# Kernel optimization log

Hardware: AMD Instinct MI355X
Metric: run time of the kernel (lower is better)

## Reference

```python
import jax, jax.numpy as jnp
import numpy as np

N, E, B = 102400, 1638400, 512
DIN, DH, DG = 64, 100, 20
D2, D3 = 200, 300
DF, R, AH, GH, H1, H2, DOUT = 64, 8, 128, 128, 128, 32, 1
EPS = 1e-5


def _xavier(k, i, o):
    lim = float(np.sqrt(6.0 / (i + o)))
    return jax.random.uniform(k, (i, o), minval=-lim, maxval=lim, dtype=jnp.float32)


def setup_inputs() -> dict:
    key = jax.random.key(0)
    ks = jax.random.split(key, 32)
    inp = {
        'node_feat': jax.random.normal(ks[0], (N, DIN), dtype=jnp.float32),
        'self_feat': jax.random.normal(ks[1], (B, D2), dtype=jnp.float32),
        'x3d': jax.random.normal(ks[2], (B, D3), dtype=jnp.float32),
        'src': jax.random.randint(ks[3], (E,), 0, N, dtype=jnp.int32),
        'dst': jax.random.randint(ks[4], (E,), 0, N, dtype=jnp.int32),
        'graph_id': (jnp.arange(N, dtype=jnp.int32) // (N // B)),
        # GCN params (weights stored (in, out))
        'gc1_w': _xavier(ks[5], DIN, DH), 'gc1_b': jnp.zeros((DH,), jnp.float32),
        'gc2_w': _xavier(ks[6], DH, DG), 'gc2_b': jnp.zeros((DG,), jnp.float32),
        # modality gate MLP
        'gate_w1': _xavier(ks[7], DG + D2 + D3, GH), 'gate_b1': jnp.zeros((GH,), jnp.float32),
        'gate_w2': _xavier(ks[8], GH, 3), 'gate_b2': jnp.zeros((3,), jnp.float32),
        # fusion projections + layernorms
        'pg_w': _xavier(ks[9], DG, DF), 'pg_b': jnp.zeros((DF,), jnp.float32),
        'p2_w': _xavier(ks[10], D2, DF), 'p2_b': jnp.zeros((DF,), jnp.float32),
        'p3_w': _xavier(ks[11], D3, DF), 'p3_b': jnp.zeros((DF,), jnp.float32),
        'lng_g': jnp.ones((DF,), jnp.float32), 'lng_b': jnp.zeros((DF,), jnp.float32),
        'ln2_g': jnp.ones((DF,), jnp.float32), 'ln2_b': jnp.zeros((DF,), jnp.float32),
        'ln3_g': jnp.ones((DF,), jnp.float32), 'ln3_b': jnp.zeros((DF,), jnp.float32),
        # low-rank CP factors
        'U_w': _xavier(ks[12], DF, R * DF),
        'V_w': _xavier(ks[13], DF, R * DF),
        'S_w': _xavier(ks[14], DF, R * DF),
        # rank attention MLP
        'attn_w1': _xavier(ks[15], DG + D2 + D3, AH), 'attn_b1': jnp.zeros((AH,), jnp.float32),
        'attn_w2': _xavier(ks[16], AH, R), 'attn_b2': jnp.zeros((R,), jnp.float32),
        # head MLP + batchnorms (training-mode batch stats)
        'fc1_w': _xavier(ks[17], DF, H1), 'fc1_b': jnp.zeros((H1,), jnp.float32),
        'fc2_w': _xavier(ks[18], H1, H2), 'fc2_b': jnp.zeros((H2,), jnp.float32),
        'fc3_w': _xavier(ks[19], H2, DOUT), 'fc3_b': jnp.zeros((DOUT,), jnp.float32),
        'bn1_g': jnp.ones((H1,), jnp.float32), 'bn1_b': jnp.zeros((H1,), jnp.float32),
        'bn2_g': jnp.ones((H2,), jnp.float32), 'bn2_b': jnp.zeros((H2,), jnp.float32),
    }
    return inp


def _gcn(h, src, dst, w, b):
    n = h.shape[0]
    msg = jax.ops.segment_sum(h[src], dst, num_segments=n)           # gather + scatter-add
    deg = jax.ops.segment_sum(jnp.ones((src.shape[0],), h.dtype), dst, num_segments=n)
    agg = msg / jnp.maximum(deg, 1.0)[:, None]                       # mean over mailbox
    return agg @ w + b


def _ln(x, g, b):
    mu = jnp.mean(x, axis=-1, keepdims=True)
    var = jnp.mean(jnp.square(x - mu), axis=-1, keepdims=True)
    return g * (x - mu) * jax.lax.rsqrt(var + EPS) + b


def _bn(x, g, b):
    mu = jnp.mean(x, axis=0)
    var = jnp.mean(jnp.square(x - mu), axis=0)
    return g * (x - mu) * jax.lax.rsqrt(var + EPS) + b


def reference(node_feat, self_feat, x3d, src, dst, graph_id,
              gc1_w, gc1_b, gc2_w, gc2_b,
              gate_w1, gate_b1, gate_w2, gate_b2,
              pg_w, pg_b, p2_w, p2_b, p3_w, p3_b,
              lng_g, lng_b, ln2_g, ln2_b, ln3_g, ln3_b,
              U_w, V_w, S_w,
              attn_w1, attn_b1, attn_w2, attn_b2,
              fc1_w, fc1_b, fc2_w, fc2_b, fc3_w, fc3_b,
              bn1_g, bn1_b, bn2_g, bn2_b):
    b = self_feat.shape[0]
    # two GCN layers (copy_u + mean reduce + linear), relu
    h = jax.nn.relu(_gcn(node_feat, src, dst, gc1_w, gc1_b))
    h = jax.nn.relu(_gcn(h, src, dst, gc2_w, gc2_b))
    # dgl.mean_nodes: per-graph mean readout
    cnt = jax.ops.segment_sum(jnp.ones((h.shape[0],), h.dtype), graph_id, num_segments=b)
    hg = jax.ops.segment_sum(h, graph_id, num_segments=b) / cnt[:, None]  # (B, DG)
    # modality gate
    cat = jnp.concatenate([hg, self_feat, x3d], axis=-1)
    alpha = jax.nn.softmax(jax.nn.relu(cat @ gate_w1 + gate_b1) @ gate_w2 + gate_b2, axis=-1)
    hg2 = hg * alpha[:, 0:1]
    sf2 = self_feat * alpha[:, 1:2]
    x3d2 = x3d * alpha[:, 2:3]
    # low-rank tri-linear fusion with rank attention (dropout = identity, eval mode)
    gp = jax.nn.relu(_ln(hg2 @ pg_w + pg_b, lng_g, lng_b))
    d2 = jax.nn.relu(_ln(sf2 @ p2_w + p2_b, ln2_g, ln2_b))
    d3 = jax.nn.relu(_ln(x3d2 @ p3_w + p3_b, ln3_g, ln3_b))
    g_r = (gp @ U_w).reshape(b, R, DF)
    d2_r = (d2 @ V_w).reshape(b, R, DF)
    d3_r = (d3 @ S_w).reshape(b, R, DF)
    z_r = g_r * d2_r * d3_r                                          # (B, R, DF)
    cat2 = jnp.concatenate([hg2, sf2, x3d2], axis=-1)
    beta = jax.nn.softmax(jax.nn.relu(cat2 @ attn_w1 + attn_b1) @ attn_w2 + attn_b2, axis=-1)
    z = jnp.sum(z_r * beta[:, :, None], axis=1)                      # (B, DF)
    # head MLP with batchnorm (batch statistics)
    out = jax.nn.relu(_bn(z @ fc1_w + fc1_b, bn1_g, bn1_b))
    out = jax.nn.relu(_bn(out @ fc2_w + fc2_b, bn2_g, bn2_b))
    out = out @ fc3_w + fc3_b
    return out
```

## Files before the change

kernel.cpp:

```cpp
#include <hip/hip_runtime.h>

#define N_NODES 102400
#define N_EDGES 1638400
#define BB 512
#define DIN 64
#define DH 100
#define DG 20
#define D2 200
#define D3 300
#define DF 64
#define RR 8
#define H1 128
#define H2 32
#define NPG (N_NODES / BB)
#define EPSV 1e-5f
#define CAP 48
#define TB6 6
#define NSLICE 8
#define SLICEN (N_NODES / NSLICE)
#define EBLK 6400
#define SEGC 64
#define PAIRS_S (EBLK * SEGC)
#define SUBN 400
#define TROWS 2

typedef float v2f __attribute__((ext_vector_type(2)));
typedef unsigned v4u __attribute__((ext_vector_type(4)));

__device__ __forceinline__ float wave_sum64(float v) {
#pragma unroll
    for (int m = 32; m >= 1; m >>= 1) v += __shfl_xor(v, m, 64);
    return v;
}

__device__ __forceinline__ unsigned enc4_fp8(float x0, float x1, float x2, float x3) {
    int r = __builtin_amdgcn_cvt_pk_fp8_f32(x0, x1, 0, false);
    r = __builtin_amdgcn_cvt_pk_fp8_f32(x2, x3, r, true);
    return (unsigned)r;
}
__device__ __forceinline__ void dec8_acc2(uint2 w, v2f* a) {
    a[0] += __builtin_amdgcn_cvt_pk_f32_fp8((int)w.x, false);
    a[1] += __builtin_amdgcn_cvt_pk_f32_fp8((int)w.x, true);
    a[2] += __builtin_amdgcn_cvt_pk_f32_fp8((int)w.y, false);
    a[3] += __builtin_amdgcn_cvt_pk_f32_fp8((int)w.y, true);
}
__device__ __forceinline__ unsigned short f2bf(float x) {
    unsigned u = __float_as_uint(x);
    u += 0x7fffu + ((u >> 16) & 1u);
    return (unsigned short)(u >> 16);
}
__device__ __forceinline__ float bf2f(unsigned u16) {
    return __uint_as_float(u16 << 16);
}

__global__ __launch_bounds__(256) void prep(
    const float* __restrict__ nf, unsigned* __restrict__ nfb,
    const int* __restrict__ src, const int* __restrict__ dst,
    unsigned* __restrict__ pairs) {
    __shared__ int binCnt[NSLICE];
    int b = blockIdx.x, t = threadIdx.x;
    if (b < 6400) {
        int i = b * 256 + t;
        float4 v = ((const float4*)nf)[i];
        nfb[i] = enc4_fp8(v.x, v.y, v.z, v.w);
    } else {
        int idx = b - 6400;
        int e = idx * 256 + t;
        int d = __builtin_nontemporal_load(&dst[e]);
        int s = __builtin_nontemporal_load(&src[e]);
        int slice = d / SLICEN;
        unsigned code = ((unsigned)(d - slice * SLICEN) << 17) | (unsigned)s;
        if (t < NSLICE) binCnt[t] = 0;
        for (int q = t; q < NSLICE * SEGC; q += 256)
            pairs[(size_t)(q >> 6) * PAIRS_S + idx * SEGC + (q & 63)] = 0xFFFFFFFFu;
        __syncthreads();
        int loc = atomicAdd(&binCnt[slice], 1);
        if (loc < SEGC)
            pairs[(size_t)slice * PAIRS_S + idx * SEGC + loc] = code;
    }
}

__global__ __launch_bounds__(1024) void bucket(
    const unsigned* __restrict__ pairs,
    int* __restrict__ counts, int* __restrict__ col) {
    __shared__ int cnt[SUBN];
    int b = blockIdx.x, t = threadIdx.x;
    int s = b & 7, j = b >> 3;
    int dlo = j * SUBN;
    int lo = s * SLICEN;
    if (t < SUBN) cnt[t] = 0;
    __syncthreads();
    const v4u* p4 = (const v4u*)(pairs + (size_t)s * PAIRS_S);
    for (int k = 0; k < PAIRS_S / 4096; k++) {
        v4u w = __builtin_nontemporal_load(&p4[k * 1024 + t]);
#pragma unroll
        for (int q = 0; q < 4; q++) {
            unsigned code = w[q];
            int dl = (int)(code >> 17);
            unsigned rel = (unsigned)(dl - dlo);
            if (rel < (unsigned)SUBN) {
                int pos = atomicAdd(&cnt[rel], 1);
                if (pos < CAP) col[(lo + dl) * CAP + pos] = (int)(code & 0x1FFFFu);
            }
        }
    }
    __syncthreads();
    if (t < SUBN) counts[lo + dlo + t] = cnt[t];
}

__global__ __launch_bounds__(512) void agg_gather(
    const unsigned* __restrict__ nfb, const int* __restrict__ counts,
    const int* __restrict__ col, unsigned short* __restrict__ aggb) {
    const uint2* nfb2 = (const uint2*)nfb;
    int t = threadIdx.x;
    int wid = t >> 6, l = t & 63;
    int h = l >> 5, hl = l & 31;
    int o = hl & 7;
    int g = hl >> 3;
    int hb = 32 * h;
    int n = blockIdx.x * 16 + wid * 2 + h;
    int cnt = counts[n]; if (cnt > CAP) cnt = CAP;
    int cmax = max(cnt, __shfl_xor(cnt, 32, 64));
    v2f a2[4];
#pragma unroll
    for (int j = 0; j < 4; j++) { a2[j].x = 0.f; a2[j].y = 0.f; }
    int idx = (hl < cnt) ? __builtin_nontemporal_load(&col[n * CAP + hl]) : 0;
    int nIt = (min(cmax, 32) + 3) >> 2;
    int m = 0;
    for (; m + 1 < nIt; m += 2) {
        int e0 = m * 4 + g, e1 = (m + 1) * 4 + g;
        int k0 = max(min(e0, cnt - 1), 0);
        int k1 = max(min(e1, cnt - 1), 0);
        int s0 = __shfl(idx, hb + k0, 64);
        int s1 = __shfl(idx, hb + k1, 64);
        uint2 v0 = nfb2[(size_t)s0 * 8 + o];
        uint2 v1 = nfb2[(size_t)s1 * 8 + o];
        if (e0 < cnt) dec8_acc2(v0, a2);
        if (e1 < cnt) dec8_acc2(v1, a2);
    }
    if (m < nIt) {
        int e0 = m * 4 + g;
        int k0 = max(min(e0, cnt - 1), 0);
        int s0 = __shfl(idx, hb + k0, 64);
        uint2 v0 = nfb2[(size_t)s0 * 8 + o];
        if (e0 < cnt) dec8_acc2(v0, a2);
    }
    if (cmax > 32) {
        int idx_hi = (hl < 16 && 32 + hl < cnt)
                   ? __builtin_nontemporal_load(&col[n * CAP + 32 + hl]) : 0;
#pragma unroll
        for (int mm2 = 0; mm2 < 4; mm2++) {
            int e = 32 + mm2 * 4 + g;
            int kk = max(min(e, cnt - 1), 0);
            int kLo = (kk < 32) ? kk : 0;
            int kHi = (kk >= 32) ? (kk - 32) : 0;
            int sL = __shfl(idx, hb + kLo, 64);
            int sH = __shfl(idx_hi, hb + kHi, 64);
            int s = (kk >= 32) ? sH : sL;
            uint2 v = nfb2[(size_t)s * 8 + o];
            if (e < cnt) dec8_acc2(v, a2);
        }
    }
#pragma unroll
    for (int mm = 8; mm <= 16; mm <<= 1) {
#pragma unroll
        for (int j = 0; j < 4; j++) {
            v2f oth;
            oth.x = __shfl_xor(a2[j].x, mm, 64);
            oth.y = __shfl_xor(a2[j].y, mm, 64);
            a2[j] += oth;
        }
    }
    if (hl < 8) {
        float inv = 1.0f / fmaxf((float)cnt, 1.0f);
        float av[8] = {a2[0].x, a2[0].y, a2[1].x, a2[1].y,
                       a2[2].x, a2[2].y, a2[3].x, a2[3].y};
        unsigned us[8];
#pragma unroll
        for (int j = 0; j < 8; j++) us[j] = (unsigned)f2bf(av[j] * inv);
        uint4 w;
        w.x = us[0] | (us[1] << 16);
        w.y = us[2] | (us[3] << 16);
        w.z = us[4] | (us[5] << 16);
        w.w = us[6] | (us[7] << 16);
        *(uint4*)(aggb + (size_t)n * 64 + 8 * hl) = w;
    }
}

__global__ __launch_bounds__(256) void w12(
    const unsigned short* __restrict__ aggb,
    const float* __restrict__ w1, const float* __restrict__ b1,
    const float* __restrict__ w2, unsigned* __restrict__ tb) {
    __shared__ float smem[64 * 101];
    int b = blockIdx.x, t = threadIdx.x;
    int n0 = b * 64;
    const uint4* ag4 = (const uint4*)(aggb + (size_t)n0 * 64);
#pragma unroll
    for (int k = 0; k < 2; k++) {
        int q = t + k * 256;
        uint4 w = ag4[q];
        int row = q >> 3, c8 = (q & 7) * 8;
        float* sa = &smem[row * 65 + c8];
        sa[0] = bf2f(w.x & 0xffffu); sa[1] = bf2f(w.x >> 16);
        sa[2] = bf2f(w.y & 0xffffu); sa[3] = bf2f(w.y >> 16);
        sa[4] = bf2f(w.z & 0xffffu); sa[5] = bf2f(w.z >> 16);
        sa[6] = bf2f(w.w & 0xffffu); sa[7] = bf2f(w.w >> 16);
    }
    __syncthreads();
    int lane = t & 63;
    int c0 = __builtin_amdgcn_readfirstlane((t >> 6) * 25);
    float acc[25];
#pragma unroll
    for (int cc = 0; cc < 25; cc++) acc[cc] = b1[c0 + cc];
    for (int i = 0; i < DIN; i++) {
        float x = smem[lane * 65 + i];
        const float* wr = &w1[i * DH + c0];
#pragma unroll
        for (int cc = 0; cc < 25; cc++) acc[cc] += x * wr[cc];
    }
    __syncthreads();
#pragma unroll
    for (int cc = 0; cc < 25; cc++)
        smem[lane * 101 + c0 + cc] = fmaxf(acc[cc], 0.f);
    __syncthreads();
    for (int task = t; task < 320; task += 256) {
        int j = task / 5, p = task % 5;
        float a0 = 0.f, a1 = 0.f, a2 = 0.f, a3 = 0.f;
        for (int i = 0; i < DH; i++) {
            float hv = smem[j * 101 + i];
            float4 w = *(const float4*)&w2[i * DG + 4 * p];
            a0 += hv * w.x; a1 += hv * w.y; a2 += hv * w.z; a3 += hv * w.w;
        }
        tb[(size_t)(n0 + j) * TB6 + p] = enc4_fp8(a0, a1, a2, a3);
    }
    if (t < 64) tb[(size_t)(n0 + t) * TB6 + 5] = 0u;
}

__global__ __launch_bounds__(512) void gcn2_gather(
    const unsigned* __restrict__ tb, const int* __restrict__ counts,
    const int* __restrict__ col,
    const float* __restrict__ b2, float* __restrict__ hg) {
    const uint2* tb2 = (const uint2*)tb;
    int t = threadIdx.x;
    int wid = t >> 6, l = t & 63;
    int h = l >> 5, hl = l & 31;
    int o = hl & 3;
    int g = hl >> 2;
    int hb = 32 * h;
    int n = blockIdx.x * 16 + wid * 2 + h;
    int cnt = counts[n]; if (cnt > CAP) cnt = CAP;
    int cmax = max(cnt, __shfl_xor(cnt, 32, 64));
    bool ok = (o < 3);
    uint2 zz = make_uint2(0u, 0u);
    v2f a2[4];
#pragma unroll
    for (int j = 0; j < 4; j++) { a2[j].x = 0.f; a2[j].y = 0.f; }
    int idx = (hl < cnt) ? __builtin_nontemporal_load(&col[n * CAP + hl]) : 0;
    int nIt = (min(cmax, 32) + 7) >> 3;
    int m = 0;
    for (; m + 1 < nIt; m += 2) {
        int e0 = m * 8 + g, e1 = (m + 1) * 8 + g;
        int k0 = max(min(e0, cnt - 1), 0);
        int k1 = max(min(e1, cnt - 1), 0);
        int s0 = __shfl(idx, hb + k0, 64);
        int s1 = __shfl(idx, hb + k1, 64);
        uint2 v0 = ok ? tb2[(size_t)s0 * 3 + o] : zz;
        uint2 v1 = ok ? tb2[(size_t)s1 * 3 + o] : zz;
        if (e0 < cnt) dec8_acc2(v0, a2);
        if (e1 < cnt) dec8_acc2(v1, a2);
    }
    if (m < nIt) {
        int e0 = m * 8 + g;
        int k0 = max(min(e0, cnt - 1), 0);
        int s0 = __shfl(idx, hb + k0, 64);
        uint2 v0 = ok ? tb2[(size_t)s0 * 3 + o] : zz;
        if (e0 < cnt) dec8_acc2(v0, a2);
    }
    if (cmax > 32) {
        int idx_hi = (hl < 16 && 32 + hl < cnt)
                   ? __builtin_nontemporal_load(&col[n * CAP + 32 + hl]) : 0;
#pragma unroll
        for (int mm2 = 0; mm2 < 2; mm2++) {
            int e = 32 + mm2 * 8 + g;
            int kk = max(min(e, cnt - 1), 0);
            int kLo = (kk < 32) ? kk : 0;
            int kHi = (kk >= 32) ? (kk - 32) : 0;
            int sL = __shfl(idx, hb + kLo, 64);
            int sH = __shfl(idx_hi, hb + kHi, 64);
            int s = (kk >= 32) ? sH : sL;
            uint2 v = ok ? tb2[(size_t)s * 3 + o] : zz;
            if (e < cnt) dec8_acc2(v, a2);
        }
    }
#pragma unroll
    for (int mm = 4; mm <= 16; mm <<= 1) {
#pragma unroll
        for (int j = 0; j < 4; j++) {
            v2f oth;
            oth.x = __shfl_xor(a2[j].x, mm, 64);
            oth.y = __shfl_xor(a2[j].y, mm, 64);
            a2[j] += oth;
        }
    }
    __shared__ float red[16][DG];
    int nb = t >> 5;
    if (hl < 3) {
        float inv = 1.0f / fmaxf((float)cnt, 1.0f);
        float av[8] = {a2[0].x, a2[0].y, a2[1].x, a2[1].y,
                       a2[2].x, a2[2].y, a2[3].x, a2[3].y};
#pragma unroll
        for (int j = 0; j < 8; j++) {
            int f = 8 * hl + j;
            if (f < DG) red[nb][f] = fmaxf(av[j] * inv + b2[f], 0.f);
        }
    }
    __syncthreads();
    if (t < 2 * DG) {
        int half = t / DG, f = t % DG;
        float s = 0.f;
#pragma unroll
        for (int j = 0; j < 8; j++) s += red[half * 8 + j][f];
        int gid = (blockIdx.x * 16 + half * 8) / NPG;
        atomicAdd(&hg[gid * DG + f], s * (1.0f / (float)NPG));
    }
}

__device__ __forceinline__ float ln_relu(float x, float g, float b) {
    float mu = wave_sum64(x) * (1.0f / DF);
    float d = x - mu;
    float var = wave_sum64(d * d) * (1.0f / DF);
    float v = g * d * rsqrtf(var + EPSV) + b;
    return fmaxf(v, 0.f);
}

__global__ __launch_bounds__(512) void row_tail(
    const float* __restrict__ hg, const float* __restrict__ sf, const float* __restrict__ x3,
    const float* __restrict__ gate_w1, const float* __restrict__ gate_b1,
    const float* __restrict__ gate_w2, const float* __restrict__ gate_b2,
    const float* __restrict__ attn_w1, const float* __restrict__ attn_b1,
    const float* __restrict__ attn_w2, const float* __restrict__ attn_b2,
    const float* __restrict__ pg_w, const float* __restrict__ pg_b,
    const float* __restrict__ p2_w, const float* __restrict__ p2_b,
    const float* __restrict__ p3_w, const float* __restrict__ p3_b,
    const float* __restrict__ lng_g, const float* __restrict__ lng_b,
    const float* __restrict__ ln2_g, const float* __restrict__ ln2_b,
    const float* __restrict__ ln3_g, const float* __restrict__ ln3_b,
    const float* __restrict__ U_w, const float* __restrict__ V_w, const float* __restrict__ S_w,
    const float* __restrict__ fc1_w, const float* __restrict__ fc1_b,
    float* __restrict__ y1) {
    int r0 = blockIdx.x * TROWS, t = threadIdx.x;
    __shared__ float s_in[TROWS][DG + D2 + D3];
    __shared__ float s_part[1024];
    __shared__ float s_hid[TROWS][128];
    __shared__ float s_sm[TROWS][RR];
    __shared__ float s_alpha[TROWS][3];
    __shared__ float s_beta[TROWS][RR];
    __shared__ float s_raw[3][TROWS][DF];
    __shared__ float s_gp[TROWS][DF], s_d2[TROWS][DF], s_d3[TROWS][DF], s_z[TROWS][DF];

    for (int q = t; q < TROWS * 520; q += 512) {
        int r = q / 520, i = q % 520;
        s_in[r][i] = (i < DG) ? hg[(r0 + r) * DG + i]
                   : (i < DG + D2) ? sf[(r0 + r) * D2 + (i - DG)]
                   : x3[(r0 + r) * D3 + (i - DG - D2)];
    }
    __syncthreads();

    {
        int c = t & 127, ks = t >> 7, k0 = ks * 130;
        float a0 = 0.f, a1 = 0.f;
        for (int i = k0; i < k0 + 130; i++) {
            float w = gate_w1[i * 128 + c];
            a0 += s_in[0][i] * w; a1 += s_in[1][i] * w;
        }
        s_part[(ks * 2 + 0) * 128 + c] = a0;
        s_part[(ks * 2 + 1) * 128 + c] = a1;
    }
    __syncthreads();
    if (t < 256) {
        int r = t >> 7, c = t & 127;
        float h = s_part[(0 + r) * 128 + c] + s_part[(2 + r) * 128 + c]
                + s_part[(4 + r) * 128 + c] + s_part[(6 + r) * 128 + c] + gate_b1[c];
        s_hid[r][c] = fmaxf(h, 0.f);
    }
    __syncthreads();
    if (t < TROWS * 3) {
        int r = t / 3, j = t % 3;
        float p = gate_b2[j];
        for (int i = 0; i < 128; i++) p += s_hid[r][i] * gate_w2[i * 3 + j];
        s_sm[r][j] = p;
    }
    __syncthreads();
    if (t < TROWS) {
        float mx = fmaxf(s_sm[t][0], fmaxf(s_sm[t][1], s_sm[t][2]));
        float e0 = __expf(s_sm[t][0] - mx), e1 = __expf(s_sm[t][1] - mx), e2 = __expf(s_sm[t][2] - mx);
        float inv = 1.0f / (e0 + e1 + e2);
        s_alpha[t][0] = e0 * inv; s_alpha[t][1] = e1 * inv; s_alpha[t][2] = e2 * inv;
    }
    __syncthreads();
    for (int q = t; q < TROWS * 520; q += 512) {
        int r = q / 520, i = q % 520;
        float sc = (i < DG) ? s_alpha[r][0] : (i < DG + D2) ? s_alpha[r][1] : s_alpha[r][2];
        s_in[r][i] *= sc;
    }
    __syncthreads();

    {
        int c = t & 127, ks = t >> 7, k0 = ks * 130;
        float a0 = 0.f, a1 = 0.f;
        for (int i = k0; i < k0 + 130; i++) {
            float w = attn_w1[i * 128 + c];
            a0 += s_in[0][i] * w; a1 += s_in[1][i] * w;
        }
        s_part[(ks * 2 + 0) * 128 + c] = a0;
        s_part[(ks * 2 + 1) * 128 + c] = a1;
    }
    __syncthreads();
    if (t < 256) {
        int r = t >> 7, c = t & 127;
        float h = s_part[(0 + r) * 128 + c] + s_part[(2 + r) * 128 + c]
                + s_part[(4 + r) * 128 + c] + s_part[(6 + r) * 128 + c] + attn_b1[c];
        s_hid[r][c] = fmaxf(h, 0.f);
    }
    __syncthreads();
    if (t < TROWS * RR) {
        int r = t / RR, j = t % RR;
        float p = attn_b2[j];
        for (int i = 0; i < 128; i++) p += s_hid[r][i] * attn_w2[i * RR + j];
        s_sm[r][j] = p;
    }
    __syncthreads();
    if (t < TROWS) {
        float mx = -1e30f;
#pragma unroll
        for (int k = 0; k < RR; k++) mx = fmaxf(mx, s_sm[t][k]);
        float se = 0.f, e[RR];
#pragma unroll
        for (int k = 0; k < RR; k++) { e[k] = __expf(s_sm[t][k] - mx); se += e[k]; }
        float inv = 1.0f / se;
#pragma unroll
        for (int k = 0; k < RR; k++) s_beta[t][k] = e[k] * inv;
    }
    if (t < TROWS * DF) {
        int r = t >> 6, c = t & 63;
        float a = pg_b[c];
        for (int i = 0; i < DG; i++) a += s_in[r][i] * pg_w[i * DF + c];
        s_raw[0][r][c] = a;
    }
    {
        int ks = t >> 6, c = t & 63, k0 = ks * 25;
        float a0 = 0.f, a1 = 0.f;
        for (int u = 0; u < 25; u++) {
            float w = p2_w[(k0 + u) * DF + c];
            a0 += s_in[0][DG + k0 + u] * w; a1 += s_in[1][DG + k0 + u] * w;
        }
        s_part[(ks * 2 + 0) * 64 + c] = a0;
        s_part[(ks * 2 + 1) * 64 + c] = a1;
    }
    __syncthreads();
    if (t < TROWS * DF) {
        int r = t >> 6, c = t & 63;
        float a = p2_b[c];
#pragma unroll
        for (int ks = 0; ks < 8; ks++) a += s_part[(ks * 2 + r) * 64 + c];
        s_raw[1][r][c] = a;
    }
    __syncthreads();
    {
        int ks = t >> 6, c = t & 63;
        int k0 = (ks * 300) >> 3, k1 = ((ks + 1) * 300) >> 3;
        float a0 = 0.f, a1 = 0.f;
        for (int i = k0; i < k1; i++) {
            float w = p3_w[i * DF + c];
            a0 += s_in[0][DG + D2 + i] * w; a1 += s_in[1][DG + D2 + i] * w;
        }
        s_part[(ks * 2 + 0) * 64 + c] = a0;
        s_part[(ks * 2 + 1) * 64 + c] = a1;
    }
    __syncthreads();
    if (t < TROWS * DF) {
        int r = t >> 6, c = t & 63;
        float a = p3_b[c];
#pragma unroll
        for (int ks = 0; ks < 8; ks++) a += s_part[(ks * 2 + r) * 64 + c];
        s_gp[r][c] = ln_relu(s_raw[0][r][c], lng_g[c], lng_b[c]);
        s_d2[r][c] = ln_relu(s_raw[1][r][c], ln2_g[c], ln2_b[c]);
        s_d3[r][c] = ln_relu(a, ln3_g[c], ln3_b[c]);
    }
    __syncthreads();

    {
        int rr = t >> 6, f = t & 63;
        float u0 = 0.f, u1 = 0.f, v0 = 0.f, v1 = 0.f, w0 = 0.f, w1 = 0.f;
        for (int i = 0; i < DF; i++) {
            float uw = U_w[i * (RR * DF) + rr * DF + f];
            float vw = V_w[i * (RR * DF) + rr * DF + f];
            float sw = S_w[i * (RR * DF) + rr * DF + f];
            u0 += s_gp[0][i] * uw; u1 += s_gp[1][i] * uw;
            v0 += s_d2[0][i] * vw; v1 += s_d2[1][i] * vw;
            w0 += s_d3[0][i] * sw; w1 += s_d3[1][i] * sw;
        }
        s_part[(rr * 2 + 0) * 64 + f] = s_beta[0][rr] * u0 * v0 * w0;
        s_part[(rr * 2 + 1) * 64 + f] = s_beta[1][rr] * u1 * v1 * w1;
    }
    __syncthreads();
    if (t < TROWS * DF) {
        int r = t >> 6, f = t & 63;
        float z = 0.f;
#pragma unroll
        for (int rr = 0; rr < 8; rr++) z += s_part[(rr * 2 + r) * 64 + f];
        s_z[r][f] = z;
    }
    __syncthreads();

    {
        int c = t & 127, ks = t >> 7, k0 = ks * 16;
        float a0 = 0.f, a1 = 0.f;
        for (int i = k0; i < k0 + 16; i++) {
            float w = fc1_w[i * H1 + c];
            a0 += s_z[0][i] * w; a1 += s_z[1][i] * w;
        }
        s_part[(ks * 2 + 0) * 128 + c] = a0;
        s_part[(ks * 2 + 1) * 128 + c] = a1;
    }
    __syncthreads();
    if (t < 256) {
        int r = t >> 7, c = t & 127;
        float a = fc1_b[c];
#pragma unroll
        for (int ks = 0; ks < 4; ks++) a += s_part[(ks * 2 + r) * 128 + c];
        y1[(r0 + r) * H1 + c] = a;
    }
}

__global__ __launch_bounds__(256) void head2(
    const float* __restrict__ y1,
    const float* __restrict__ bn1_g, const float* __restrict__ bn1_b,
    const float* __restrict__ fc2_w, const float* __restrict__ fc2_b,
    float* __restrict__ y2) {
    int row = blockIdx.x, t = threadIdx.x;
    __shared__ float sp[2][H1], sp2[2][H1];
    int h = t >> 7, c = t & 127;
    float s = 0.f, s2 = 0.f;
#pragma unroll 8
    for (int r = h * 256; r < h * 256 + 256; r++) {
        float v = y1[r * H1 + c];
        s += v; s2 += v * v;
    }
    sp[h][c] = s; sp2[h][c] = s2;
    __syncthreads();
    __shared__ float sh[H1];
    if (t < H1) {
        float S = sp[0][t] + sp[1][t];
        float S2 = sp2[0][t] + sp2[1][t];
        float m = S * (1.0f / BB);
        float ri = rsqrtf(S2 * (1.0f / BB) - m * m + EPSV);
        float v = y1[row * H1 + t];
        sh[t] = fmaxf(bn1_g[t] * (v - m) * ri + bn1_b[t], 0.f);
    }
    __syncthreads();
    if (t < H2) {
        float acc = fc2_b[t];
        for (int i = 0; i < H1; i++) acc += sh[i] * fc2_w[i * H2 + t];
        y2[row * H2 + t] = acc;
    }
}

__global__ __launch_bounds__(256) void head3(
    const float* __restrict__ y2,
    const float* __restrict__ bn2_g, const float* __restrict__ bn2_b,
    const float* __restrict__ fc3_w, const float* __restrict__ fc3_b,
    float* __restrict__ out) {
    int t = threadIdx.x;
    __shared__ float smu[H2], sri[H2];
    if (t < H2) {
        float s = 0.f, s2 = 0.f;
#pragma unroll 8
        for (int r = 0; r < BB; r++) {
            float v = y2[r * H2 + t];
            s += v; s2 += v * v;
        }
        float m = s * (1.0f / BB);
        smu[t] = m;
        sri[t] = rsqrtf(s2 * (1.0f / BB) - m * m + EPSV);
    }
    __syncthreads();
    int row = blockIdx.x * 256 + t;
    float acc = fc3_b[0];
    for (int i = 0; i < H2; i++) {
        float v = y2[row * H2 + i];
        v = bn2_g[i] * (v - smu[i]) * sri[i] + bn2_b[i];
        acc += fmaxf(v, 0.f) * fc3_w[i];
    }
    out[row] = acc;
}

extern "C" void kernel_launch(void* const* d_in, const int* in_sizes, int n_in,
                              void* d_out, int out_size, void* d_ws, size_t ws_size,
                              hipStream_t stream) {
    const float* node_feat = (const float*)d_in[0];
    const float* self_feat = (const float*)d_in[1];
    const float* x3d       = (const float*)d_in[2];
    const int*   src       = (const int*)d_in[3];
    const int*   dst       = (const int*)d_in[4];
    const float* gc1_w = (const float*)d_in[6];
    const float* gc1_b = (const float*)d_in[7];
    const float* gc2_w = (const float*)d_in[8];
    const float* gc2_b = (const float*)d_in[9];
    const float* gate_w1 = (const float*)d_in[10];
    const float* gate_b1 = (const float*)d_in[11];
    const float* gate_w2 = (const float*)d_in[12];
    const float* gate_b2 = (const float*)d_in[13];
    const float* pg_w = (const float*)d_in[14];
    const float* pg_b = (const float*)d_in[15];
    const float* p2_w = (const float*)d_in[16];
    const float* p2_b = (const float*)d_in[17];
    const float* p3_w = (const float*)d_in[18];
    const float* p3_b = (const float*)d_in[19];
    const float* lng_g = (const float*)d_in[20];
    const float* lng_b = (const float*)d_in[21];
    const float* ln2_g = (const float*)d_in[22];
    const float* ln2_b = (const float*)d_in[23];
    const float* ln3_g = (const float*)d_in[24];
    const float* ln3_b = (const float*)d_in[25];
    const float* U_w = (const float*)d_in[26];
    const float* V_w = (const float*)d_in[27];
    const float* S_w = (const float*)d_in[28];
    const float* attn_w1 = (const float*)d_in[29];
    const float* attn_b1 = (const float*)d_in[30];
    const float* attn_w2 = (const float*)d_in[31];
    const float* attn_b2 = (const float*)d_in[32];
    const float* fc1_w = (const float*)d_in[33];
    const float* fc1_b = (const float*)d_in[34];
    const float* fc2_w = (const float*)d_in[35];
    const float* fc2_b = (const float*)d_in[36];
    const float* fc3_w = (const float*)d_in[37];
    const float* fc3_b = (const float*)d_in[38];
    const float* bn1_g = (const float*)d_in[39];
    const float* bn1_b = (const float*)d_in[40];
    const float* bn2_g = (const float*)d_in[41];
    const float* bn2_b = (const float*)d_in[42];

    char* base = (char*)d_ws;
    int* counts   = (int*)base;                      base += sizeof(int) * N_NODES;
    int* col      = (int*)base;                      base += sizeof(int) * (size_t)N_NODES * CAP;
    unsigned* nfb = (unsigned*)base;                 base += sizeof(unsigned) * (size_t)N_NODES * 16;
    unsigned* tb  = (unsigned*)base;                 base += sizeof(unsigned) * (size_t)N_NODES * TB6;
    unsigned short* aggb = (unsigned short*)base;    base += sizeof(unsigned short) * (size_t)N_NODES * 64;
    float* hg    = (float*)base;                     base += sizeof(float) * BB * DG;
    float* y1    = (float*)base;                     base += sizeof(float) * BB * H1;
    float* y2    = (float*)base;                     base += sizeof(float) * BB * H2;
    float* outf  = (float*)d_out;
    unsigned* pairs = (unsigned*)aggb;

    hipMemsetAsync(hg, 0, sizeof(float) * BB * DG, stream);

    prep<<<6400 + EBLK, 256, 0, stream>>>(node_feat, nfb, src, dst, pairs);
    bucket<<<256, 1024, 0, stream>>>(pairs, counts, col);

    agg_gather<<<N_NODES / 16, 512, 0, stream>>>(nfb, counts, col, aggb);
    w12<<<N_NODES / 64, 256, 0, stream>>>(aggb, gc1_w, gc1_b, gc2_w, tb);
    gcn2_gather<<<N_NODES / 16, 512, 0, stream>>>(tb, counts, col, gc2_b, hg);

    row_tail<<<BB / TROWS, 512, 0, stream>>>(hg, self_feat, x3d,
                                     gate_w1, gate_b1, gate_w2, gate_b2,
                                     attn_w1, attn_b1, attn_w2, attn_b2,
                                     pg_w, pg_b, p2_w, p2_b, p3_w, p3_b,
                                     lng_g, lng_b, ln2_g, ln2_b, ln3_g, ln3_b,
                                     U_w, V_w, S_w, fc1_w, fc1_b, y1);
    head2<<<BB, 256, 0, stream>>>(y1, bn1_g, bn1_b, fc2_w, fc2_b, y2);
    head3<<<BB / 256, 256, 0, stream>>>(y2, bn2_g, bn2_b, fc3_w, fc3_b, outf);
}
```

Before: 413.5 us.

## Split bucket pass across pair halves and widen row_tail to 1024 threads

The bucket kernel now has each block handle 800 destination nodes over half of the edge-pair stream. The two halves fill col from opposite ends and merge their counts with packed 16-bit atomics into a zeroed counts array. The gather kernels unpack the two counts and remap slots around the gap between them. row_tail moves to 1024 threads with finer K splits so each block does less serial work per thread. The cost is an extra memset, the atomics, and extra index arithmetic in the gathers.

```diff
diff --git a/kernel.cpp b/kernel.cpp
--- a/kernel.cpp
+++ b/kernel.cpp
@@ -21,7 +21,7 @@
 #define EBLK 6400
 #define SEGC 64
 #define PAIRS_S (EBLK * SEGC)
-#define SUBN 400
+#define SUBN 800
 #define TROWS 2
 
 typedef float v2f __attribute__((ext_vector_type(2)));
@@ -51,6 +51,14 @@
 }
 __device__ __forceinline__ float bf2f(unsigned u16) {
     return __uint_as_float(u16 << 16);
+}
+
+__device__ __forceinline__ void cnt_unpack(int w, int& cnt0, int& cnt) {
+    cnt0 = w & 0xffff;
+    int cnt1 = (w >> 16) & 0xffff;
+    if (cnt0 > CAP) cnt0 = CAP;
+    if (cnt1 > CAP - cnt0) cnt1 = CAP - cnt0;
+    cnt = cnt0 + cnt1;
 }
 
 __global__ __launch_bounds__(256) void prep(
@@ -85,13 +93,15 @@
     int* __restrict__ counts, int* __restrict__ col) {
     __shared__ int cnt[SUBN];
     int b = blockIdx.x, t = threadIdx.x;
-    int s = b & 7, j = b >> 3;
+    int s = b & 7;
+    int u = b >> 3;
+    int j = u & 15, h = u >> 4;
     int dlo = j * SUBN;
     int lo = s * SLICEN;
-    if (t < SUBN) cnt[t] = 0;
-    __syncthreads();
-    const v4u* p4 = (const v4u*)(pairs + (size_t)s * PAIRS_S);
-    for (int k = 0; k < PAIRS_S / 4096; k++) {
+    for (int q = t; q < SUBN; q += 1024) cnt[q] = 0;
+    __syncthreads();
+    const v4u* p4 = (const v4u*)(pairs + (size_t)s * PAIRS_S + (size_t)h * (PAIRS_S / 2));
+    for (int k = 0; k < (PAIRS_S / 2) / 4096; k++) {
         v4u w = __builtin_nontemporal_load(&p4[k * 1024 + t]);
 #pragma unroll
         for (int q = 0; q < 4; q++) {
@@ -100,12 +110,16 @@
             unsigned rel = (unsigned)(dl - dlo);
             if (rel < (unsigned)SUBN) {
                 int pos = atomicAdd(&cnt[rel], 1);
-                if (pos < CAP) col[(lo + dl) * CAP + pos] = (int)(code & 0x1FFFFu);
+                if (pos < CAP) {
+                    int slot = h ? (CAP - 1 - pos) : pos;
+                    col[(lo + dl) * CAP + slot] = (int)(code & 0x1FFFFu);
+                }
             }
         }
     }
     __syncthreads();
-    if (t < SUBN) counts[lo + dlo + t] = cnt[t];
+    for (int q = t; q < SUBN; q += 1024)
+        atomicAdd(&counts[lo + dlo + q], cnt[q] << (16 * h));
 }
 
 __global__ __launch_bounds__(512) void agg_gather(
@@ -119,12 +133,15 @@
     int g = hl >> 3;
     int hb = 32 * h;
     int n = blockIdx.x * 16 + wid * 2 + h;
-    int cnt = counts[n]; if (cnt > CAP) cnt = CAP;
+    int cnt0, cnt;
+    cnt_unpack(counts[n], cnt0, cnt);
+    int gap = CAP - cnt;
     int cmax = max(cnt, __shfl_xor(cnt, 32, 64));
     v2f a2[4];
 #pragma unroll
     for (int j = 0; j < 4; j++) { a2[j].x = 0.f; a2[j].y = 0.f; }
-    int idx = (hl < cnt) ? __builtin_nontemporal_load(&col[n * CAP + hl]) : 0;
+    int slot0 = (hl < cnt0) ? hl : hl + gap;
+    int idx = (hl < cnt) ? __builtin_nontemporal_load(&col[n * CAP + slot0]) : 0;
     int nIt = (min(cmax, 32) + 3) >> 2;
     int m = 0;
     for (; m + 1 < nIt; m += 2) {
@@ -146,8 +163,10 @@
         if (e0 < cnt) dec8_acc2(v0, a2);
     }
     if (cmax > 32) {
-        int idx_hi = (hl < 16 && 32 + hl < cnt)
-                   ? __builtin_nontemporal_load(&col[n * CAP + 32 + hl]) : 0;
+        int e32 = 32 + hl;
+        int slotH = (e32 < cnt0) ? e32 : e32 + gap;
+        int idx_hi = (hl < 16 && e32 < cnt)
+                   ? __builtin_nontemporal_load(&col[n * CAP + slotH]) : 0;
 #pragma unroll
         for (int mm2 = 0; mm2 < 4; mm2++) {
             int e = 32 + mm2 * 4 + g;
@@ -248,14 +267,17 @@
     int g = hl >> 2;
     int hb = 32 * h;
     int n = blockIdx.x * 16 + wid * 2 + h;
-    int cnt = counts[n]; if (cnt > CAP) cnt = CAP;
+    int cnt0, cnt;
+    cnt_unpack(counts[n], cnt0, cnt);
+    int gap = CAP - cnt;
     int cmax = max(cnt, __shfl_xor(cnt, 32, 64));
     bool ok = (o < 3);
     uint2 zz = make_uint2(0u, 0u);
     v2f a2[4];
 #pragma unroll
     for (int j = 0; j < 4; j++) { a2[j].x = 0.f; a2[j].y = 0.f; }
-    int idx = (hl < cnt) ? __builtin_nontemporal_load(&col[n * CAP + hl]) : 0;
+    int slot0 = (hl < cnt0) ? hl : hl + gap;
+    int idx = (hl < cnt) ? __builtin_nontemporal_load(&col[n * CAP + slot0]) : 0;
     int nIt = (min(cmax, 32) + 7) >> 3;
     int m = 0;
     for (; m + 1 < nIt; m += 2) {
@@ -277,8 +299,10 @@
         if (e0 < cnt) dec8_acc2(v0, a2);
     }
     if (cmax > 32) {
-        int idx_hi = (hl < 16 && 32 + hl < cnt)
-                   ? __builtin_nontemporal_load(&col[n * CAP + 32 + hl]) : 0;
+        int e32 = 32 + hl;
+        int slotH = (e32 < cnt0) ? e32 : e32 + gap;
+        int idx_hi = (hl < 16 && e32 < cnt)
+                   ? __builtin_nontemporal_load(&col[n * CAP + slotH]) : 0;
 #pragma unroll
         for (int mm2 = 0; mm2 < 2; mm2++) {
             int e = 32 + mm2 * 8 + g;
@@ -333,7 +357,7 @@
     return fmaxf(v, 0.f);
 }
 
-__global__ __launch_bounds__(512) void row_tail(
+__global__ __launch_bounds__(1024) void row_tail(
     const float* __restrict__ hg, const float* __restrict__ sf, const float* __restrict__ x3,
     const float* __restrict__ gate_w1, const float* __restrict__ gate_b1,
     const float* __restrict__ gate_w2, const float* __restrict__ gate_b2,
@@ -350,15 +374,15 @@
     float* __restrict__ y1) {
     int r0 = blockIdx.x * TROWS, t = threadIdx.x;
     __shared__ float s_in[TROWS][DG + D2 + D3];
-    __shared__ float s_part[1024];
+    __shared__ float s_part[2048];
     __shared__ float s_hid[TROWS][128];
     __shared__ float s_sm[TROWS][RR];
     __shared__ float s_alpha[TROWS][3];
     __shared__ float s_beta[TROWS][RR];
-    __shared__ float s_raw[3][TROWS][DF];
+    __shared__ float s_raw[2][TROWS][DF];
     __shared__ float s_gp[TROWS][DF], s_d2[TROWS][DF], s_d3[TROWS][DF], s_z[TROWS][DF];
 
-    for (int q = t; q < TROWS * 520; q += 512) {
+    for (int q = t; q < TROWS * 520; q += 1024) {
         int r = q / 520, i = q % 520;
         s_in[r][i] = (i < DG) ? hg[(r0 + r) * DG + i]
                    : (i < DG + D2) ? sf[(r0 + r) * D2 + (i - DG)]
@@ -367,9 +391,9 @@
     __syncthreads();
 
     {
-        int c = t & 127, ks = t >> 7, k0 = ks * 130;
+        int c = t & 127, ks = t >> 7, k0 = ks * 65;
         float a0 = 0.f, a1 = 0.f;
-        for (int i = k0; i < k0 + 130; i++) {
+        for (int i = k0; i < k0 + 65; i++) {
             float w = gate_w1[i * 128 + c];
             a0 += s_in[0][i] * w; a1 += s_in[1][i] * w;
         }
@@ -379,9 +403,10 @@
     __syncthreads();
     if (t < 256) {
         int r = t >> 7, c = t & 127;
-        float h = s_part[(0 + r) * 128 + c] + s_part[(2 + r) * 128 + c]
-                + s_part[(4 + r) * 128 + c] + s_part[(6 + r) * 128 + c] + gate_b1[c];
-        s_hid[r][c] = fmaxf(h, 0.f);
+        float hsum = gate_b1[c];
+#pragma unroll
+        for (int ks = 0; ks < 8; ks++) hsum += s_part[(ks * 2 + r) * 128 + c];
+        s_hid[r][c] = fmaxf(hsum, 0.f);
     }
     __syncthreads();
     if (t < TROWS * 3) {
@@ -398,7 +423,7 @@
         s_alpha[t][0] = e0 * inv; s_alpha[t][1] = e1 * inv; s_alpha[t][2] = e2 * inv;
     }
     __syncthreads();
-    for (int q = t; q < TROWS * 520; q += 512) {
+    for (int q = t; q < TROWS * 520; q += 1024) {
         int r = q / 520, i = q % 520;
         float sc = (i < DG) ? s_alpha[r][0] : (i < DG + D2) ? s_alpha[r][1] : s_alpha[r][2];
         s_in[r][i] *= sc;
@@ -406,9 +431,9 @@
     __syncthreads();
 
     {
-        int c = t & 127, ks = t >> 7, k0 = ks * 130;
+        int c = t & 127, ks = t >> 7, k0 = ks * 65;
         float a0 = 0.f, a1 = 0.f;
-        for (int i = k0; i < k0 + 130; i++) {
+        for (int i = k0; i < k0 + 65; i++) {
             float w = attn_w1[i * 128 + c];
             a0 += s_in[0][i] * w; a1 += s_in[1][i] * w;
         }
@@ -418,9 +443,10 @@
     __syncthreads();
     if (t < 256) {
         int r = t >> 7, c = t & 127;
-        float h = s_part[(0 + r) * 128 + c] + s_part[(2 + r) * 128 + c]
-                + s_part[(4 + r) * 128 + c] + s_part[(6 + r) * 128 + c] + attn_b1[c];
-        s_hid[r][c] = fmaxf(h, 0.f);
+        float hsum = attn_b1[c];
+#pragma unroll
+        for (int ks = 0; ks < 8; ks++) hsum += s_part[(ks * 2 + r) * 128 + c];
+        s_hid[r][c] = fmaxf(hsum, 0.f);
     }
     __syncthreads();
     if (t < TROWS * RR) {
@@ -448,11 +474,12 @@
         s_raw[0][r][c] = a;
     }
     {
-        int ks = t >> 6, c = t & 63, k0 = ks * 25;
+        int ks = t >> 6, c = t & 63;
+        int k0 = (ks * 200) >> 4, k1 = ((ks + 1) * 200) >> 4;
         float a0 = 0.f, a1 = 0.f;
-        for (int u = 0; u < 25; u++) {
-            float w = p2_w[(k0 + u) * DF + c];
-            a0 += s_in[0][DG + k0 + u] * w; a1 += s_in[1][DG + k0 + u] * w;
+        for (int i = k0; i < k1; i++) {
+            float w = p2_w[i * DF + c];
+            a0 += s_in[0][DG + i] * w; a1 += s_in[1][DG + i] * w;
         }
         s_part[(ks * 2 + 0) * 64 + c] = a0;
         s_part[(ks * 2 + 1) * 64 + c] = a1;
@@ -462,13 +489,13 @@
         int r = t >> 6, c = t & 63;
         float a = p2_b[c];
 #pragma unroll
-        for (int ks = 0; ks < 8; ks++) a += s_part[(ks * 2 + r) * 64 + c];
+        for (int ks = 0; ks < 16; ks++) a += s_part[(ks * 2 + r) * 64 + c];
         s_raw[1][r][c] = a;
     }
     __syncthreads();
     {
         int ks = t >> 6, c = t & 63;
-        int k0 = (ks * 300) >> 3, k1 = ((ks + 1) * 300) >> 3;
+        int k0 = (ks * 300) >> 4, k1 = ((ks + 1) * 300) >> 4;
         float a0 = 0.f, a1 = 0.f;
         for (int i = k0; i < k1; i++) {
             float w = p3_w[i * DF + c];
@@ -482,7 +509,7 @@
         int r = t >> 6, c = t & 63;
         float a = p3_b[c];
 #pragma unroll
-        for (int ks = 0; ks < 8; ks++) a += s_part[(ks * 2 + r) * 64 + c];
+        for (int ks = 0; ks < 16; ks++) a += s_part[(ks * 2 + r) * 64 + c];
         s_gp[r][c] = ln_relu(s_raw[0][r][c], lng_g[c], lng_b[c]);
         s_d2[r][c] = ln_relu(s_raw[1][r][c], ln2_g[c], ln2_b[c]);
         s_d3[r][c] = ln_relu(a, ln3_g[c], ln3_b[c]);
@@ -490,18 +517,14 @@
     __syncthreads();
 
     {
-        int rr = t >> 6, f = t & 63;
-        float u0 = 0.f, u1 = 0.f, v0 = 0.f, v1 = 0.f, w0 = 0.f, w1 = 0.f;
+        int row = t >> 9, rr = (t >> 6) & 7, f = t & 63;
+        float gu = 0.f, dv = 0.f, ds = 0.f;
         for (int i = 0; i < DF; i++) {
-            float uw = U_w[i * (RR * DF) + rr * DF + f];
-            float vw = V_w[i * (RR * DF) + rr * DF + f];
-            float sw = S_w[i * (RR * DF) + rr * DF + f];
-            u0 += s_gp[0][i] * uw; u1 += s_gp[1][i] * uw;
-            v0 += s_d2[0][i] * vw; v1 += s_d2[1][i] * vw;
-            w0 += s_d3[0][i] * sw; w1 += s_d3[1][i] * sw;
-        }
-        s_part[(rr * 2 + 0) * 64 + f] = s_beta[0][rr] * u0 * v0 * w0;
-        s_part[(rr * 2 + 1) * 64 + f] = s_beta[1][rr] * u1 * v1 * w1;
+            gu += s_gp[row][i] * U_w[i * (RR * DF) + rr * DF + f];
+            dv += s_d2[row][i] * V_w[i * (RR * DF) + rr * DF + f];
+            ds += s_d3[row][i] * S_w[i * (RR * DF) + rr * DF + f];
+        }
+        s_part[(rr * 2 + row) * 64 + f] = s_beta[row][rr] * gu * dv * ds;
     }
     __syncthreads();
     if (t < TROWS * DF) {
@@ -514,9 +537,9 @@
     __syncthreads();
 
     {
-        int c = t & 127, ks = t >> 7, k0 = ks * 16;
+        int c = t & 127, ks = t >> 7, k0 = ks * 8;
         float a0 = 0.f, a1 = 0.f;
-        for (int i = k0; i < k0 + 16; i++) {
+        for (int i = k0; i < k0 + 8; i++) {
             float w = fc1_w[i * H1 + c];
             a0 += s_z[0][i] * w; a1 += s_z[1][i] * w;
         }
@@ -528,7 +551,7 @@
         int r = t >> 7, c = t & 127;
         float a = fc1_b[c];
 #pragma unroll
-        for (int ks = 0; ks < 4; ks++) a += s_part[(ks * 2 + r) * 128 + c];
+        for (int ks = 0; ks < 8; ks++) a += s_part[(ks * 2 + r) * 128 + c];
         y1[(r0 + r) * H1 + c] = a;
     }
 }
@@ -653,6 +676,7 @@
     float* outf  = (float*)d_out;
     unsigned* pairs = (unsigned*)aggb;
 
+    hipMemsetAsync(counts, 0, sizeof(int) * N_NODES, stream);
     hipMemsetAsync(hg, 0, sizeof(float) * BB * DG, stream);
 
     prep<<<6400 + EBLK, 256, 0, stream>>>(node_feat, nfb, src, dst, pairs);
@@ -662,7 +686,7 @@
     w12<<<N_NODES / 64, 256, 0, stream>>>(aggb, gc1_w, gc1_b, gc2_w, tb);
     gcn2_gather<<<N_NODES / 16, 512, 0, stream>>>(tb, counts, col, gc2_b, hg);
 
-    row_tail<<<BB / TROWS, 512, 0, stream>>>(hg, self_feat, x3d,
+    row_tail<<<BB / TROWS, 1024, 0, stream>>>(hg, self_feat, x3d,
                                      gate_w1, gate_b1, gate_w2, gate_b2,
                                      attn_w1, attn_b1, attn_w2, attn_b2,
                                      pg_w, pg_b, p2_w, p2_b, p3_w, p3_b,
```

Result: no change. 407.7 us (-1.4%).

## Split bucket pass into two half-scans per slice with packed counts

Applied to the files above, without the earlier changes.

The bucket kernel now covers 800 destinations per block and splits each slice's pair stream into two halves, handled by separate blocks. The first half fills column slots from the front and the second from the back, and each half's count goes into 16 bits of a packed counter merged with atomics. The gather kernels unpack both counts and remap slot indices around the gap. This halves the number of times each pair segment is re-read across blocks (from 16 to 8 scans per slice) while keeping the same block count. In exchange it needs a memset of the counts buffer, global atomics, and extra index arithmetic in both gathers.

```diff
diff --git a/kernel.cpp b/kernel.cpp
--- a/kernel.cpp
+++ b/kernel.cpp
@@ -21,7 +21,7 @@
 #define EBLK 6400
 #define SEGC 64
 #define PAIRS_S (EBLK * SEGC)
-#define SUBN 400
+#define SUBN 800
 #define TROWS 2
 
 typedef float v2f __attribute__((ext_vector_type(2)));
@@ -51,6 +51,14 @@
 }
 __device__ __forceinline__ float bf2f(unsigned u16) {
     return __uint_as_float(u16 << 16);
+}
+
+__device__ __forceinline__ void cnt_unpack(int w, int& cnt0, int& cnt) {
+    cnt0 = w & 0xffff;
+    int cnt1 = (w >> 16) & 0xffff;
+    if (cnt0 > CAP) cnt0 = CAP;
+    if (cnt1 > CAP - cnt0) cnt1 = CAP - cnt0;
+    cnt = cnt0 + cnt1;
 }
 
 __global__ __launch_bounds__(256) void prep(
@@ -85,13 +93,15 @@
     int* __restrict__ counts, int* __restrict__ col) {
     __shared__ int cnt[SUBN];
     int b = blockIdx.x, t = threadIdx.x;
-    int s = b & 7, j = b >> 3;
+    int s = b & 7;
+    int u = b >> 3;
+    int j = u & 15, h = u >> 4;
     int dlo = j * SUBN;
     int lo = s * SLICEN;
-    if (t < SUBN) cnt[t] = 0;
-    __syncthreads();
-    const v4u* p4 = (const v4u*)(pairs + (size_t)s * PAIRS_S);
-    for (int k = 0; k < PAIRS_S / 4096; k++) {
+    for (int q = t; q < SUBN; q += 1024) cnt[q] = 0;
+    __syncthreads();
+    const v4u* p4 = (const v4u*)(pairs + (size_t)s * PAIRS_S + (size_t)h * (PAIRS_S / 2));
+    for (int k = 0; k < (PAIRS_S / 2) / 4096; k++) {
         v4u w = __builtin_nontemporal_load(&p4[k * 1024 + t]);
 #pragma unroll
         for (int q = 0; q < 4; q++) {
@@ -100,12 +110,16 @@
             unsigned rel = (unsigned)(dl - dlo);
             if (rel < (unsigned)SUBN) {
                 int pos = atomicAdd(&cnt[rel], 1);
-                if (pos < CAP) col[(lo + dl) * CAP + pos] = (int)(code & 0x1FFFFu);
+                if (pos < CAP) {
+                    int slot = h ? (CAP - 1 - pos) : pos;
+                    col[(lo + dl) * CAP + slot] = (int)(code & 0x1FFFFu);
+                }
             }
         }
     }
     __syncthreads();
-    if (t < SUBN) counts[lo + dlo + t] = cnt[t];
+    for (int q = t; q < SUBN; q += 1024)
+        atomicAdd(&counts[lo + dlo + q], cnt[q] << (16 * h));
 }
 
 __global__ __launch_bounds__(512) void agg_gather(
@@ -119,12 +133,15 @@
     int g = hl >> 3;
     int hb = 32 * h;
     int n = blockIdx.x * 16 + wid * 2 + h;
-    int cnt = counts[n]; if (cnt > CAP) cnt = CAP;
+    int cnt0, cnt;
+    cnt_unpack(counts[n], cnt0, cnt);
+    int gap = CAP - cnt;
     int cmax = max(cnt, __shfl_xor(cnt, 32, 64));
     v2f a2[4];
 #pragma unroll
     for (int j = 0; j < 4; j++) { a2[j].x = 0.f; a2[j].y = 0.f; }
-    int idx = (hl < cnt) ? __builtin_nontemporal_load(&col[n * CAP + hl]) : 0;
+    int slot0 = (hl < cnt0) ? hl : hl + gap;
+    int idx = (hl < cnt) ? __builtin_nontemporal_load(&col[n * CAP + slot0]) : 0;
     int nIt = (min(cmax, 32) + 3) >> 2;
     int m = 0;
     for (; m + 1 < nIt; m += 2) {
@@ -146,8 +163,10 @@
         if (e0 < cnt) dec8_acc2(v0, a2);
     }
     if (cmax > 32) {
-        int idx_hi = (hl < 16 && 32 + hl < cnt)
-                   ? __builtin_nontemporal_load(&col[n * CAP + 32 + hl]) : 0;
+        int e32 = 32 + hl;
+        int slotH = (e32 < cnt0) ? e32 : e32 + gap;
+        int idx_hi = (hl < 16 && e32 < cnt)
+                   ? __builtin_nontemporal_load(&col[n * CAP + slotH]) : 0;
 #pragma unroll
         for (int mm2 = 0; mm2 < 4; mm2++) {
             int e = 32 + mm2 * 4 + g;
@@ -248,14 +267,17 @@
     int g = hl >> 2;
     int hb = 32 * h;
     int n = blockIdx.x * 16 + wid * 2 + h;
-    int cnt = counts[n]; if (cnt > CAP) cnt = CAP;
+    int cnt0, cnt;
+    cnt_unpack(counts[n], cnt0, cnt);
+    int gap = CAP - cnt;
     int cmax = max(cnt, __shfl_xor(cnt, 32, 64));
     bool ok = (o < 3);
     uint2 zz = make_uint2(0u, 0u);
     v2f a2[4];
 #pragma unroll
     for (int j = 0; j < 4; j++) { a2[j].x = 0.f; a2[j].y = 0.f; }
-    int idx = (hl < cnt) ? __builtin_nontemporal_load(&col[n * CAP + hl]) : 0;
+    int slot0 = (hl < cnt0) ? hl : hl + gap;
+    int idx = (hl < cnt) ? __builtin_nontemporal_load(&col[n * CAP + slot0]) : 0;
     int nIt = (min(cmax, 32) + 7) >> 3;
     int m = 0;
     for (; m + 1 < nIt; m += 2) {
@@ -277,8 +299,10 @@
         if (e0 < cnt) dec8_acc2(v0, a2);
     }
     if (cmax > 32) {
-        int idx_hi = (hl < 16 && 32 + hl < cnt)
-                   ? __builtin_nontemporal_load(&col[n * CAP + 32 + hl]) : 0;
+        int e32 = 32 + hl;
+        int slotH = (e32 < cnt0) ? e32 : e32 + gap;
+        int idx_hi = (hl < 16 && e32 < cnt)
+                   ? __builtin_nontemporal_load(&col[n * CAP + slotH]) : 0;
 #pragma unroll
         for (int mm2 = 0; mm2 < 2; mm2++) {
             int e = 32 + mm2 * 8 + g;
@@ -355,7 +379,7 @@
     __shared__ float s_sm[TROWS][RR];
     __shared__ float s_alpha[TROWS][3];
     __shared__ float s_beta[TROWS][RR];
-    __shared__ float s_raw[3][TROWS][DF];
+    __shared__ float s_raw[2][TROWS][DF];
     __shared__ float s_gp[TROWS][DF], s_d2[TROWS][DF], s_d3[TROWS][DF], s_z[TROWS][DF];
 
     for (int q = t; q < TROWS * 520; q += 512) {
@@ -653,6 +677,7 @@
     float* outf  = (float*)d_out;
     unsigned* pairs = (unsigned*)aggb;
 
+    hipMemsetAsync(counts, 0, sizeof(int) * N_NODES, stream);
     hipMemsetAsync(hg, 0, sizeof(float) * BB * DG, stream);
 
     prep<<<6400 + EBLK, 256, 0, stream>>>(node_feat, nfb, src, dst, pairs);
```

Result: faster. 402.6 us (-2.6%).
